# Kernel tuning notes

Hardware: AMD Instinct MI355X
Metric: run time of the kernel (lower is better)

Reference implementation:

```python
import jax, jax.numpy as jnp
from jax import lax
import numpy as np

B, N, C = 16, 2048, 512


def setup_inputs() -> dict:
    key = jax.random.key(0)
    ks = jax.random.split(key, 9)
    s1 = (2.0 / C) ** 0.5   # kaiming fan_in for k=1 convs
    s3 = (2.0 / (3 * C)) ** 0.5  # kaiming fan_in for k=3 convs
    return {
        "x": jax.random.normal(ks[0], (B, N, C), jnp.float32),
        "w1_q": jax.random.normal(ks[1], (C, C), jnp.float32) * s1,
        "w3_q": jax.random.normal(ks[2], (C, C, 3), jnp.float32) * s3,
        "w1_k": jax.random.normal(ks[3], (C, C), jnp.float32) * s1,
        "w3_k": jax.random.normal(ks[4], (C, C, 3), jnp.float32) * s3,
        "w1_v": jax.random.normal(ks[5], (C, C), jnp.float32) * s1,
        "w3_v": jax.random.normal(ks[6], (C, C, 3), jnp.float32) * s3,
        "w_proj": jax.random.normal(ks[7], (C, C), jnp.float32) * s1,
        "b_proj": jax.random.normal(ks[8], (C,), jnp.float32) * 0.01,
    }


def _qkv_branch(xc, w1, w3):
    # xc: [B, C, N]; conv1d k=1 (no bias) then conv1d k=3, circular pad 1 (no bias)
    h = jnp.einsum("oc,bcn->bon", w1, xc)
    hp = jnp.pad(h, ((0, 0), (0, 0), (1, 1)), mode="wrap")
    return lax.conv_general_dilated(
        hp, w3, window_strides=(1,), padding="VALID",
        dimension_numbers=("NCH", "OIH", "NCH"))  # [B, C, N]


def reference(x, w1_q, w3_q, w1_k, w3_k, w1_v, w3_v, w_proj, b_proj):
    # x: [B, N, C]
    xc = jnp.transpose(x, (0, 2, 1))  # [B, C, N]
    q = _qkv_branch(xc, w1_q, w3_q)
    k = _qkv_branch(xc, w1_k, w3_k)
    v = _qkv_branch(xc, w1_v, w3_v)
    # channel attention: scores are [B, C, C]; scale applied twice = 1/d_model
    scale2 = 1.0 / C
    attn = jnp.einsum("bcn,bdn->bcd", q, k) * scale2
    attn = jax.nn.softmax(attn, axis=-1)
    out = jnp.einsum("bcd,bdn->bcn", attn, v)  # [B, C, N]
    y = jnp.einsum("oc,bcn->bon", w_proj, out) + b_proj[None, :, None]
    return jnp.transpose(y, (0, 2, 1))  # [B, N, C]
```

## Files before the change

### kernel.cpp

```cpp
#include <hip/hip_runtime.h>
#include <hip/hip_bf16.h>
#include <hip/hip_fp16.h>
#include <stdint.h>

typedef __bf16 bf16;
typedef __bf16 bf16x8 __attribute__((ext_vector_type(8)));
typedef _Float16 f16x8 __attribute__((ext_vector_type(8)));
typedef float f32x4 __attribute__((ext_vector_type(4)));

#define NSEQ 2048
#define CDIM 512

#define WS_FLAGS   0
#define WS_BPB     1024
#define WS_WPB     4096
#define WS_WEC     532480
#define WS_WECT    3678208
#define WS_W1T     5251072
#define WS_W3R     6823936
#define WS_BASE    11542528

__device__ __forceinline__ float rdf(const void* p, long i, int f) {
  if (f == 1) return ((const float*)p)[i];
  if (f == 2) return (float)((const _Float16*)p)[i];
  return (float)((const bf16*)p)[i];
}

__device__ __forceinline__ void gl_lds16(const bf16* g, bf16* l) {
  __builtin_amdgcn_global_load_lds(
      (__attribute__((address_space(1))) void*)g,
      (__attribute__((address_space(3))) void*)l, 16, 0, 0);
}

__device__ __forceinline__ void stage_one(const void* gb, long eoff, int dt,
                                          bf16* ldst)
{
  if (dt == 1) {
    const float* g = (const float*)gb + eoff;
    const float4 u0 = *(const float4*)g;
    const float4 u1 = *(const float4*)(g + 4);
    bf16x8 t;
    t[0]=(bf16)u0.x; t[1]=(bf16)u0.y; t[2]=(bf16)u0.z; t[3]=(bf16)u0.w;
    t[4]=(bf16)u1.x; t[5]=(bf16)u1.y; t[6]=(bf16)u1.z; t[7]=(bf16)u1.w;
    *(bf16x8*)ldst = t;
  } else if (dt == 2) {
    const f16x8 h = *(const f16x8*)((const _Float16*)gb + eoff);
    bf16x8 t;
#pragma unroll
    for (int j = 0; j < 8; ++j) t[j] = (bf16)(float)h[j];
    *(bf16x8*)ldst = t;
  } else {
    gl_lds16((const bf16*)gb + eoff, ldst);
  }
}

__global__ __launch_bounds__(256)
void detect2(const unsigned short* __restrict__ a,
             const unsigned short* __restrict__ b, int* __restrict__ flags)
{
  const unsigned short* p = blockIdx.x ? b : a;
  __shared__ int chi, clo;
  if (threadIdx.x == 0) { chi = 0; clo = 0; }
  __syncthreads();
  int hi = 0, lo = 0;
  for (int i = threadIdx.x; i < 4096; i += 256) {
    const int e = (p[i] >> 7) & 0xff;
    hi += (e >= 141);
    lo += (e >= 1 && e <= 110);
  }
  atomicAdd(&chi, hi);
  atomicAdd(&clo, lo);
  __syncthreads();
  if (threadIdx.x == 0) {
    flags[blockIdx.x] = (chi > 8) ? 1 : ((clo > 100) ? 2 : 0);
    if (blockIdx.x == 0) flags[2] = 0;
  }
}

__global__ __launch_bounds__(256)
void cvt_x8(const void* __restrict__ x, const int* __restrict__ flag,
            bf16* __restrict__ xb)
{
  const long i8 = (long)blockIdx.x * 256 + threadIdx.x;
  const int f = *flag;
  bf16x8 t;
  if (f == 1) {
    const float4* g = (const float4*)x + i8 * 2;
    const float4 u0 = g[0], u1 = g[1];
    t[0]=(bf16)u0.x; t[1]=(bf16)u0.y; t[2]=(bf16)u0.z; t[3]=(bf16)u0.w;
    t[4]=(bf16)u1.x; t[5]=(bf16)u1.y; t[6]=(bf16)u1.z; t[7]=(bf16)u1.w;
  } else if (f == 2) {
    const f16x8 h = ((const f16x8*)x)[i8];
#pragma unroll
    for (int j = 0; j < 8; ++j) t[j] = (bf16)(float)h[j];
  } else {
    t = ((const bf16x8*)x)[i8];
  }
  ((bf16x8*)xb)[i8] = t;
}

template<int AX3, int BX3, int EPI, int ZMODE>
__global__ __launch_bounds__(256)
void gemm_bt(const void* __restrict__ Abase, const void* __restrict__ Bbase,
             void* __restrict__ Cbase, const bf16* __restrict__ bias,
             const int* __restrict__ xflag, int zxb,
             int M, int Nd, int K, int lda, int ldb, int ldc,
             long zsA, long zsB, long zsC)
{
  __shared__ bf16 As[128 * 32];
  __shared__ bf16 Bs[128 * 32];
  const int z = blockIdx.z;
  const int xdt = (AX3 || BX3) ? *xflag : 0;
  long Aoff, Boff; char* CB;
  if (ZMODE == 1) {
    const int g = z / 3, t = z - g * 3;
    Aoff = (long)z * 262144;
    Boff = (long)g * 262144;
    CB = (char*)Cbase + ((long)g * (512 * 1536) + t * 512) * 2;
  } else {
    Aoff = AX3 ? 0 : (long)z * zsA;
    Boff = BX3 ? 0 : (long)z * zsB;
    CB = (char*)Cbase + (long)z * zsC * (EPI == 2 ? 4 : 2);
  }
  const int m0 = blockIdx.y * 128;
  const int n0 = blockIdx.x * 128;
  const int tid = threadIdx.x;
  const int lane = tid & 63;
  const int w = tid >> 6;
  const int wr = (w >> 1) * 64;
  const int wc = (w & 1) * 64;

  f32x4 acc[4][4];
  const f32x4 zero = {0.f, 0.f, 0.f, 0.f};
#pragma unroll
  for (int i = 0; i < 4; ++i)
#pragma unroll
    for (int j = 0; j < 4; ++j) acc[i][j] = zero;

  for (int k0 = 0; k0 < K; k0 += 32) {
#pragma unroll
    for (int it = 0; it < 2; ++it) {
      const int f  = (it * 256 + tid) * 16;
      const int r  = f >> 6;
      const int cb = (f & 63) >> 1;
      long ea, eb;
      if (AX3) {
        const int tau = k0 >> 9;
        ea = (long)(z + zxb) * zsA +
             (long)((m0 + r + tau - 1) & (NSEQ - 1)) * CDIM + (k0 & 511) + cb;
      } else {
        ea = Aoff + (long)(m0 + r) * lda + k0 + cb;
      }
      stage_one(Abase, ea, AX3 ? xdt : 0, (bf16*)((char*)As + f));
      if (BX3) {
        const int tau = k0 >> 9;
        eb = (long)(z + zxb) * zsB +
             (long)((n0 + r + tau - 1) & (NSEQ - 1)) * CDIM + (k0 & 511) + cb;
      } else {
        eb = Boff + (long)(n0 + r) * ldb + k0 + cb;
      }
      stage_one(Bbase, eb, BX3 ? xdt : 0, (bf16*)((char*)Bs + f));
    }
    __syncthreads();

    const int qb = (lane >> 4) * 16;
    const int fr = lane & 15;
    bf16x8 af[4], bfr[4];
#pragma unroll
    for (int i = 0; i < 4; ++i)
      af[i] = *(const bf16x8*)((const char*)As + (wr + i * 16 + fr) * 64 + qb);
#pragma unroll
    for (int j = 0; j < 4; ++j)
      bfr[j] = *(const bf16x8*)((const char*)Bs + (wc + j * 16 + fr) * 64 + qb);
#pragma unroll
    for (int i = 0; i < 4; ++i)
#pragma unroll
      for (int j = 0; j < 4; ++j)
        acc[i][j] = __builtin_amdgcn_mfma_f32_16x16x32_bf16(af[i], bfr[j], acc[i][j], 0, 0, 0);
    __syncthreads();
  }

  const int qa4 = (lane >> 4) * 4;
  const int cn = lane & 15;
#pragma unroll
  for (int i = 0; i < 4; ++i) {
#pragma unroll
    for (int j = 0; j < 4; ++j) {
      const int gn = n0 + wc + j * 16 + cn;
      const float bv = (EPI == 2) ? (float)bias[gn] : 0.f;
#pragma unroll
      for (int r = 0; r < 4; ++r) {
        const long gm = m0 + wr + i * 16 + qa4 + r;
        if (EPI == 2) ((float*)CB)[gm * ldc + gn] = acc[i][j][r] + bv;
        else          ((bf16*)CB)[gm * ldc + gn] = (bf16)acc[i][j][r];
      }
    }
  }
}

template<int X3>
__device__ __forceinline__ void stage32(const bf16* __restrict__ gb, long zoff,
                                        int r0, int k0, int ld,
                                        char* ldsb, int tid)
{
#pragma unroll
  for (int is = 0; is < 2; ++is) {
    const int c = is * 512 + tid;
    const int g = c >> 6;
    const int l = c & 63;
    const int r = g * 16 + (l & 15);
    const int kb = l >> 4;
    long e;
    if (X3) {
      const int tau = k0 >> 9;
      const int rg = (r0 + r + tau - 1) & (NSEQ - 1);
      e = zoff + (long)rg * CDIM + ((k0 & 511) + kb * 8);
    } else {
      e = zoff + (long)(r0 + r) * ld + k0 + kb * 8;
    }
    gl_lds16(gb + e, (bf16*)(ldsb + c * 16));
  }
}

template<int AX3, int BX3, int EPI>
__global__ __launch_bounds__(512)
void gemm8(const bf16* __restrict__ Ab, const bf16* __restrict__ Bb,
           void* __restrict__ Cbase, const bf16* __restrict__ bias,
           int zxb, int M, int Nd, int K, int lda, int ldb, int ldc,
           long zsA, long zsB, long zsC)
{
  __shared__ char smem[65536];
  const int z = blockIdx.z;
  const long Aoff = (long)(AX3 ? (z + zxb) : z) * zsA;
  const long Boff = (long)(BX3 ? (z + zxb) : z) * zsB;
  char* CB = (char*)Cbase + (long)z * zsC * (EPI == 2 ? 4 : 2);
  const int m0 = blockIdx.y * 256;
  const int n0 = blockIdx.x * 256;
  const int tid = threadIdx.x;
  const int lane = tid & 63;
  const int w = tid >> 6, wm = w >> 2, wn = w & 3;
  const int fro = lane * 16;

  f32x4 acc[8][4];
  const f32x4 zero = {0.f, 0.f, 0.f, 0.f};
#pragma unroll
  for (int i = 0; i < 8; ++i)
#pragma unroll
    for (int j = 0; j < 4; ++j) acc[i][j] = zero;

  const int KT = K >> 5;
  stage32<AX3>(Ab, Aoff, m0, 0, lda, smem, tid);
  stage32<BX3>(Bb, Boff, n0, 0, ldb, smem + 16384, tid);
  __syncthreads();

  for (int T = 0; T < KT; ++T) {
    const int cur = T & 1;
    const char* sA = smem + cur * 32768;
    const char* sB = sA + 16384;
    if (T + 1 < KT) {
      char* nb = smem + (cur ^ 1) * 32768;
      const int k1 = (T + 1) << 5;
      stage32<AX3>(Ab, Aoff, m0, k1, lda, nb, tid);
      stage32<BX3>(Bb, Boff, n0, k1, ldb, nb + 16384, tid);
    }
    bf16x8 bfr[4];
#pragma unroll
    for (int j = 0; j < 4; ++j)
      bfr[j] = *(const bf16x8*)(sB + (wn * 4 + j) * 1024 + fro);
#pragma unroll
    for (int h = 0; h < 2; ++h) {
      bf16x8 af[4];
#pragma unroll
      for (int i2 = 0; i2 < 4; ++i2)
        af[i2] = *(const bf16x8*)(sA + (wm * 8 + h * 4 + i2) * 1024 + fro);
      __builtin_amdgcn_s_setprio(1);
#pragma unroll
      for (int i2 = 0; i2 < 4; ++i2)
#pragma unroll
        for (int j = 0; j < 4; ++j)
          acc[h * 4 + i2][j] = __builtin_amdgcn_mfma_f32_16x16x32_bf16(
              af[i2], bfr[j], acc[h * 4 + i2][j], 0, 0, 0);
      __builtin_amdgcn_s_setprio(0);
      if (h == 0) __builtin_amdgcn_s_barrier();
    }
    __syncthreads();
  }

  const int lr = lane & 15, lk = lane >> 4;
#pragma unroll
  for (int i = 0; i < 8; ++i) {
#pragma unroll
    for (int j = 0; j < 4; ++j) {
      const int gn = n0 + wn * 64 + j * 16 + lr;
      const float bv = (EPI == 2) ? (float)bias[gn] : 0.f;
#pragma unroll
      for (int r = 0; r < 4; ++r) {
        const long gm = m0 + wm * 128 + i * 16 + lk * 4 + r;
        if (EPI == 2) ((float*)CB)[gm * ldc + gn] = acc[i][j][r] + bv;
        else          ((bf16*)CB)[gm * ldc + gn] = (bf16)acc[i][j][r];
      }
    }
  }
}

template<int AX3, int BX3, int EPI>
__global__ __launch_bounds__(512)
void gemm8p(const bf16* __restrict__ Ab, const bf16* __restrict__ Bb,
            void* __restrict__ Cbase, const bf16* __restrict__ bias,
            int zxb, int M, int Nd, int K, int lda, int ldb, int ldc,
            long zsA, long zsB, long zsC)
{
  extern __shared__ char smem[];
  const int gx = gridDim.x, gy = gridDim.y;
  const int total = gx * gy * gridDim.z;
  const int lin = blockIdx.x + gx * (blockIdx.y + gy * blockIdx.z);
  const int q = total >> 3, r = total & 7;
  const int xcd = lin & 7, k = lin >> 3;
  int swz = (xcd < r ? xcd * (q + 1) : r * (q + 1) + (xcd - r) * q) + k;
  const int ny = swz % gy; swz /= gy;
  const int nx = swz % gx;
  const int z  = swz / gx;

  const long Aoff = (long)(AX3 ? (z + zxb) : z) * zsA;
  const long Boff = (long)(BX3 ? (z + zxb) : z) * zsB;
  char* CB = (char*)Cbase + (long)z * zsC * (EPI == 2 ? 4 : 2);
  const int m0 = ny * 256;
  const int n0 = nx * 256;
  const int tid = threadIdx.x;
  const int lane = tid & 63;
  const int w = tid >> 6, wm = w >> 2, wn = w & 3;
  const int fro = lane * 16;

  f32x4 acc[8][4];
  const f32x4 zero = {0.f, 0.f, 0.f, 0.f};
#pragma unroll
  for (int i = 0; i < 8; ++i)
#pragma unroll
    for (int j = 0; j < 4; ++j) acc[i][j] = zero;

  const int KT = K >> 5;

  stage32<AX3>(Ab, Aoff, m0, 0, lda, smem, tid);
  stage32<BX3>(Bb, Boff, n0, 0, ldb, smem + 16384, tid);
  stage32<AX3>(Ab, Aoff, m0, 32, lda, smem + 32768, tid);
  stage32<BX3>(Bb, Boff, n0, 32, ldb, smem + 32768 + 16384, tid);

  for (int T = 0; T < KT; ++T) {
    if (T + 1 < KT) asm volatile("s_waitcnt vmcnt(4)" ::: "memory");
    else            asm volatile("s_waitcnt vmcnt(0)" ::: "memory");
    __builtin_amdgcn_s_barrier();

    if (T + 2 < KT) {
      char* nb = smem + ((T + 2) % 3) * 32768;
      const int k2 = (T + 2) << 5;
      stage32<AX3>(Ab, Aoff, m0, k2, lda, nb, tid);
      stage32<BX3>(Bb, Boff, n0, k2, ldb, nb + 16384, tid);
    }

    const char* sA = smem + (T % 3) * 32768;
    const char* sB = sA + 16384;
    bf16x8 bfr[4];
#pragma unroll
    for (int j = 0; j < 4; ++j)
      bfr[j] = *(const bf16x8*)(sB + (wn * 4 + j) * 1024 + fro);
#pragma unroll
    for (int h = 0; h < 2; ++h) {
      bf16x8 af[4];
#pragma unroll
      for (int i2 = 0; i2 < 4; ++i2)
        af[i2] = *(const bf16x8*)(sA + (wm * 8 + h * 4 + i2) * 1024 + fro);
      __builtin_amdgcn_s_setprio(1);
#pragma unroll
      for (int i2 = 0; i2 < 4; ++i2)
#pragma unroll
        for (int j = 0; j < 4; ++j)
          acc[h * 4 + i2][j] = __builtin_amdgcn_mfma_f32_16x16x32_bf16(
              af[i2], bfr[j], acc[h * 4 + i2][j], 0, 0, 0);
      __builtin_amdgcn_s_setprio(0);
      if (h == 0) __builtin_amdgcn_s_barrier();
    }
  }

  const int lr = lane & 15, lk = lane >> 4;
#pragma unroll
  for (int i = 0; i < 8; ++i) {
#pragma unroll
    for (int j = 0; j < 4; ++j) {
      const int gn = n0 + wn * 64 + j * 16 + lr;
      const float bv = (EPI == 2) ? (float)bias[gn] : 0.f;
#pragma unroll
      for (int r2 = 0; r2 < 4; ++r2) {
        const long gm = m0 + wm * 128 + i * 16 + lk * 4 + r2;
        if (EPI == 2) ((float*)CB)[gm * ldc + gn] = acc[i][j][r2] + bv;
        else          ((bf16*)CB)[gm * ldc + gn] = (bf16)acc[i][j][r2];
      }
    }
  }
}

__global__ __launch_bounds__(256)
void repack(const void* __restrict__ w1q, const void* __restrict__ w3q,
            const void* __restrict__ w1k, const void* __restrict__ w3k,
            const void* __restrict__ w1v, const void* __restrict__ w3v,
            const void* __restrict__ wp, const void* __restrict__ bpr,
            const int* __restrict__ flag,
            bf16* __restrict__ w1t, bf16* __restrict__ w3r,
            bf16* __restrict__ wpb, bf16* __restrict__ bpb)
{
  const int isf = *flag;
  const int g = blockIdx.z;
  const void* w1 = (g == 0) ? w1q : (g == 1) ? w1k : w1v;
  const void* w3 = (g == 0) ? w3q : (g == 1) ? w3k : w3v;
  const int idx = blockIdx.x * 256 + threadIdx.x;
  const int o = idx >> 9, c = idx & 511;
  w1t[g * 262144 + idx] = (bf16)rdf(w1, (long)c * 512 + o, isf);
#pragma unroll
  for (int t = 0; t < 3; ++t)
    w3r[(g * 3 + t) * 262144 + idx] = (bf16)rdf(w3, ((long)o * 512 + c) * 3 + t, isf);
  if (g == 0) {
    wpb[idx] = (bf16)rdf(wp, idx, isf);
    if (idx < 512) bpb[idx] = (bf16)rdf(bpr, idx, isf);
  }
}

__global__ __launch_bounds__(256)
void softmax_p1(const bf16* __restrict__ S, float2* __restrict__ P)
{
  const int z = blockIdx.z;
  const int c = blockIdx.x * 256 + threadIdx.x;
  const int d0 = blockIdx.y * 128;
  const bf16* s = S + (long)z * 262144 + c;
  const float sc = 1.0f / 512.0f;
  float m = -3.4e38f, l = 0.f;
  for (int d = d0; d < d0 + 128; ++d) {
    const float v = (float)s[d * 512] * sc;
    const float nm = fmaxf(m, v);
    l = l * __expf(m - nm) + __expf(v - nm);
    m = nm;
  }
  P[((long)z * 4 + blockIdx.y) * 512 + c] = make_float2(m, l);
}

__global__ __launch_bounds__(256)
void softmax_p2(bf16* __restrict__ S, const float2* __restrict__ P)
{
  const int z = blockIdx.z;
  const int c = blockIdx.x * 256 + threadIdx.x;
  const int d0 = blockIdx.y * 128;
  float m = -3.4e38f, l = 0.f;
#pragma unroll
  for (int i = 0; i < 4; ++i) {
    const float2 p = P[((long)z * 4 + i) * 512 + c];
    const float nm = fmaxf(m, p.x);
    l = l * __expf(m - nm) + p.y * __expf(p.x - nm);
    m = nm;
  }
  const float inv = 1.0f / l;
  bf16* s = S + (long)z * 262144 + c;
  const float sc = 1.0f / 512.0f;
  for (int d = d0; d < d0 + 128; ++d) {
    const float v = (float)s[d * 512] * sc;
    s[d * 512] = (bf16)(__expf(v - m) * inv);
  }
}

extern "C" void kernel_launch(void* const* d_in, const int* in_sizes, int n_in,
                              void* d_out, int out_size, void* d_ws, size_t ws_size,
                              hipStream_t stream)
{
  long smax = -1, smin = (long)1 << 62;
  for (int i = 0; i < n_in; ++i) {
    const long s = in_sizes[i];
    if (s > smax) smax = s;
    if (s < smin) smin = s;
  }
  long s3 = -1;
  for (int i = 0; i < n_in; ++i) {
    const long s = in_sizes[i];
    if (s < smax && s > s3) s3 = s;
  }
  int xi = -1, bi = -1, w1i[8], n1 = 0, w3i[8], n3 = 0;
  for (int i = 0; i < n_in; ++i) {
    const long s = in_sizes[i];
    if (s == smax && xi < 0) xi = i;
    else if (s == smin && bi < 0) bi = i;
    else if (s == s3) { if (n3 < 8) w3i[n3++] = i; }
    else             { if (n1 < 8) w1i[n1++] = i; }
  }
  const void *x, *w1q, *w3q, *w1k, *w3k, *w1v, *w3v, *wp, *bp;
  if (xi >= 0 && bi >= 0 && n1 >= 4 && n3 >= 3) {
    x = d_in[xi]; bp = d_in[bi];
    w1q = d_in[w1i[0]]; w1k = d_in[w1i[1]]; w1v = d_in[w1i[2]]; wp = d_in[w1i[3]];
    w3q = d_in[w3i[0]]; w3k = d_in[w3i[1]]; w3v = d_in[w3i[2]];
  } else {
    x = d_in[0]; w1q = d_in[1]; w3q = d_in[2]; w1k = d_in[3]; w3k = d_in[4];
    w1v = d_in[5]; w3v = d_in[6]; wp = d_in[7]; bp = d_in[8];
  }
  float* out = (float*)d_out;

  char* ws = (char*)d_ws;
  int*  flags = (int*)(ws + WS_FLAGS);
  bf16* bpb  = (bf16*)(ws + WS_BPB);
  bf16* wpb  = (bf16*)(ws + WS_WPB);
  bf16* wec  = (bf16*)(ws + WS_WEC);
  bf16* wecT = (bf16*)(ws + WS_WECT);
  bf16* w1t  = (bf16*)(ws + WS_W1T);
  bf16* w3r  = (bf16*)(ws + WS_W3R);

  int NB = 16, conv = 1;
  while (NB >= 1 && WS_BASE + (size_t)NB * 2621440 + 33554432 > ws_size) NB >>= 1;
  if (NB == 0) {
    conv = 0; NB = 16;
    while (NB > 1 && WS_BASE + (size_t)NB * 2621440 > ws_size) NB >>= 1;
  }
  bf16* Sb    = (bf16*)(ws + WS_BASE);
  bf16* slotA = (bf16*)(ws + WS_BASE + (size_t)NB * 524288);
  bf16* U     = slotA;
  bf16* Wfin  = slotA + (size_t)NB * 262144;
  bf16* xb    = (bf16*)(ws + WS_BASE + (size_t)NB * 2621440);
  float2* Pp  = (float2*)slotA;

  const dim3 blk(256, 1, 1);
  const dim3 blk8(512, 1, 1);

  bool ok8 = true;
  {
    hipError_t e;
    e = hipFuncSetAttribute(reinterpret_cast<const void*>(&gemm8p<0, 1, 0>),
                            hipFuncAttributeMaxDynamicSharedMemorySize, 98304);
    ok8 = ok8 && (e == hipSuccess);
    e = hipFuncSetAttribute(reinterpret_cast<const void*>(&gemm8p<0, 0, 0>),
                            hipFuncAttributeMaxDynamicSharedMemorySize, 98304);
    ok8 = ok8 && (e == hipSuccess);
    e = hipFuncSetAttribute(reinterpret_cast<const void*>(&gemm8p<1, 0, 2>),
                            hipFuncAttributeMaxDynamicSharedMemorySize, 98304);
    ok8 = ok8 && (e == hipSuccess);
  }

  detect2<<<dim3(2, 1, 1), blk, 0, stream>>>(
      (const unsigned short*)x, (const unsigned short*)w1q, flags);

  const void* xu = x;
  const int* xflag = flags;
  if (conv) {
    cvt_x8<<<dim3(8192, 1, 1), blk, 0, stream>>>(x, flags, xb);
    xu = xb;
    xflag = flags + 2;
  }

  repack<<<dim3(1024, 1, 3), blk, 0, stream>>>(w1q, w3q, w1k, w3k, w1v, w3v,
                                               wp, bp, flags + 1,
                                               w1t, w3r, wpb, bpb);
  gemm_bt<0, 0, 0, 1><<<dim3(4, 4, 6), blk, 0, stream>>>(
      w3r, w1t, wec, nullptr, nullptr, 0, 512, 512, 512, 512, 512, 1536, 0, 0, 0);
  gemm_bt<0, 0, 0, 0><<<dim3(4, 4, 3), blk, 0, stream>>>(
      w1t + 2 * 262144, w3r + 6 * 262144, wecT, nullptr, nullptr, 0,
      512, 512, 512, 512, 512, 512, 0, 262144, 262144);

  for (int b0 = 0; b0 < 16; b0 += NB) {
    char* outc = (char*)out + (size_t)b0 * 2048 * 512 * 4;
    if (conv) {
      bf16* QKc = (bf16*)outc;
      if (ok8) {
        gemm8p<0, 1, 0><<<dim3(8, 4, NB), blk8, 98304, stream>>>(
            wec, (const bf16*)xu, QKc, nullptr, b0,
            1024, 2048, 1536, 1536, 0, 2048,
            0, (long)NSEQ * CDIM, (long)1024 * 2048);
      } else {
        gemm8<0, 1, 0><<<dim3(8, 4, NB), blk8, 0, stream>>>(
            wec, (const bf16*)xu, QKc, nullptr, b0,
            1024, 2048, 1536, 1536, 0, 2048,
            0, (long)NSEQ * CDIM, (long)1024 * 2048);
      }
      gemm_bt<0, 0, 0, 0><<<dim3(4, 4, NB), blk, 0, stream>>>(
          QKc + (long)512 * 2048, QKc, Sb, nullptr, nullptr, 0,
          512, 512, 2048, 2048, 2048, 512,
          (long)1024 * 2048, (long)1024 * 2048, (long)512 * 512);
      softmax_p1<<<dim3(2, 4, NB), blk, 0, stream>>>(Sb, Pp);
      softmax_p2<<<dim3(2, 4, NB), blk, 0, stream>>>(Sb, Pp);
      gemm_bt<0, 0, 0, 0><<<dim3(4, 4, NB), blk, 0, stream>>>(
          wpb, Sb, U, nullptr, nullptr, 0, 512, 512, 512, 512, 512, 512,
          0, (long)512 * 512, (long)512 * 512);
      if (ok8) {
        gemm8p<0, 0, 0><<<dim3(6, 2, NB), blk8, 98304, stream>>>(
            U, wecT, Wfin, nullptr, 0, 512, 1536, 512, 512, 512, 1536,
            (long)512 * 512, 0, (long)512 * 1536);
        gemm8p<1, 0, 2><<<dim3(2, 8, NB), blk8, 98304, stream>>>(
            (const bf16*)xu, Wfin, outc, bpb, b0,
            2048, 512, 1536, 0, 1536, 512,
            (long)NSEQ * CDIM, (long)512 * 1536, (long)2048 * 512);
      } else {
        gemm8<0, 0, 0><<<dim3(6, 2, NB), blk8, 0, stream>>>(
            U, wecT, Wfin, nullptr, 0, 512, 1536, 512, 512, 512, 1536,
            (long)512 * 512, 0, (long)512 * 1536);
        gemm8<1, 0, 2><<<dim3(2, 8, NB), blk8, 0, stream>>>(
            (const bf16*)xu, Wfin, outc, bpb, b0,
            2048, 512, 1536, 0, 1536, 512,
            (long)NSEQ * CDIM, (long)512 * 1536, (long)2048 * 512);
      }
    } else {
      bf16* Kc = (bf16*)outc;
      gemm_bt<0, 1, 0, 0><<<dim3(16, 4, NB), blk, 0, stream>>>(
          wec, xu, slotA, nullptr, xflag, b0, 512, 2048, 1536, 1536, 0, 2048,
          0, (long)NSEQ * CDIM, (long)512 * 2048);
      gemm_bt<0, 1, 0, 0><<<dim3(16, 4, NB), blk, 0, stream>>>(
          wec + 512 * 1536, xu, Kc, nullptr, xflag, b0, 512, 2048, 1536, 1536, 0, 2048,
          0, (long)NSEQ * CDIM, (long)512 * 2048);
      gemm_bt<0, 0, 0, 0><<<dim3(4, 4, NB), blk, 0, stream>>>(
          Kc, slotA, Sb, nullptr, nullptr, 0, 512, 512, 2048, 2048, 2048, 512,
          (long)512 * 2048, (long)512 * 2048, (long)512 * 512);
      softmax_p1<<<dim3(2, 4, NB), blk, 0, stream>>>(Sb, Pp);
      softmax_p2<<<dim3(2, 4, NB), blk, 0, stream>>>(Sb, Pp);
      gemm_bt<0, 0, 0, 0><<<dim3(4, 4, NB), blk, 0, stream>>>(
          wpb, Sb, U, nullptr, nullptr, 0, 512, 512, 512, 512, 512, 512,
          0, (long)512 * 512, (long)512 * 512);
      gemm_bt<0, 0, 0, 0><<<dim3(12, 4, NB), blk, 0, stream>>>(
          U, wecT, Wfin, nullptr, nullptr, 0, 512, 1536, 512, 512, 512, 1536,
          (long)512 * 512, 0, (long)512 * 1536);
      gemm_bt<1, 0, 2, 0><<<dim3(4, 16, NB), blk, 0, stream>>>(
          xu, Wfin, outc, bpb, xflag, b0,
          2048, 512, 1536, 0, 1536, 512,
          (long)NSEQ * CDIM, (long)512 * 1536, (long)2048 * 512);
    }
  }
}
```

Measured before the change: 437.9 us.

## Switch swizzled GEMM to 32x32x16 MFMA with matching LDS staging layout

```diff
diff --git a/kernel.cpp b/kernel.cpp
--- a/kernel.cpp
+++ b/kernel.cpp
@@ -7,6 +7,7 @@
 typedef __bf16 bf16x8 __attribute__((ext_vector_type(8)));
 typedef _Float16 f16x8 __attribute__((ext_vector_type(8)));
 typedef float f32x4 __attribute__((ext_vector_type(4)));
+typedef float f32x16 __attribute__((ext_vector_type(16)));
 
 #define NSEQ 2048
 #define CDIM 512
@@ -222,6 +223,28 @@
   }
 }
 
+template<int X3>
+__device__ __forceinline__ void stage32w(const bf16* __restrict__ gb, long zoff,
+                                         int r0, int k0, int ld,
+                                         char* ldsb, int tid)
+{
+#pragma unroll
+  for (int is = 0; is < 2; ++is) {
+    const int c = is * 512 + tid;
+    const int r = ((c >> 7) << 5) | (c & 31);
+    const int kb = (c >> 5) & 3;
+    long e;
+    if (X3) {
+      const int tau = k0 >> 9;
+      const int rg = (r0 + r + tau - 1) & (NSEQ - 1);
+      e = zoff + (long)rg * CDIM + ((k0 & 511) + kb * 8);
+    } else {
+      e = zoff + (long)(r0 + r) * ld + k0 + kb * 8;
+    }
+    gl_lds16(gb + e, (bf16*)(ldsb + c * 16));
+  }
+}
+
 template<int AX3, int BX3, int EPI>
 __global__ __launch_bounds__(512)
 void gemm8(const bf16* __restrict__ Ab, const bf16* __restrict__ Bb,
@@ -331,19 +354,20 @@
   const int w = tid >> 6, wm = w >> 2, wn = w & 3;
   const int fro = lane * 16;
 
-  f32x4 acc[8][4];
-  const f32x4 zero = {0.f, 0.f, 0.f, 0.f};
-#pragma unroll
-  for (int i = 0; i < 8; ++i)
-#pragma unroll
-    for (int j = 0; j < 4; ++j) acc[i][j] = zero;
+  f32x16 acc[4][2];
+#pragma unroll
+  for (int i = 0; i < 4; ++i)
+#pragma unroll
+    for (int j = 0; j < 2; ++j)
+#pragma unroll
+      for (int e = 0; e < 16; ++e) acc[i][j][e] = 0.f;
 
   const int KT = K >> 5;
 
-  stage32<AX3>(Ab, Aoff, m0, 0, lda, smem, tid);
-  stage32<BX3>(Bb, Boff, n0, 0, ldb, smem + 16384, tid);
-  stage32<AX3>(Ab, Aoff, m0, 32, lda, smem + 32768, tid);
-  stage32<BX3>(Bb, Boff, n0, 32, ldb, smem + 32768 + 16384, tid);
+  stage32w<AX3>(Ab, Aoff, m0, 0, lda, smem, tid);
+  stage32w<BX3>(Bb, Boff, n0, 0, ldb, smem + 16384, tid);
+  stage32w<AX3>(Ab, Aoff, m0, 32, lda, smem + 32768, tid);
+  stage32w<BX3>(Bb, Boff, n0, 32, ldb, smem + 32768 + 16384, tid);
 
   for (int T = 0; T < KT; ++T) {
     if (T + 1 < KT) asm volatile("s_waitcnt vmcnt(4)" ::: "memory");
@@ -353,46 +377,49 @@
     if (T + 2 < KT) {
       char* nb = smem + ((T + 2) % 3) * 32768;
       const int k2 = (T + 2) << 5;
-      stage32<AX3>(Ab, Aoff, m0, k2, lda, nb, tid);
-      stage32<BX3>(Bb, Boff, n0, k2, ldb, nb + 16384, tid);
+      stage32w<AX3>(Ab, Aoff, m0, k2, lda, nb, tid);
+      stage32w<BX3>(Bb, Boff, n0, k2, ldb, nb + 16384, tid);
     }
 
     const char* sA = smem + (T % 3) * 32768;
     const char* sB = sA + 16384;
-    bf16x8 bfr[4];
-#pragma unroll
-    for (int j = 0; j < 4; ++j)
-      bfr[j] = *(const bf16x8*)(sB + (wn * 4 + j) * 1024 + fro);
-#pragma unroll
-    for (int h = 0; h < 2; ++h) {
-      bf16x8 af[4];
-#pragma unroll
-      for (int i2 = 0; i2 < 4; ++i2)
-        af[i2] = *(const bf16x8*)(sA + (wm * 8 + h * 4 + i2) * 1024 + fro);
-      __builtin_amdgcn_s_setprio(1);
-#pragma unroll
-      for (int i2 = 0; i2 < 4; ++i2)
-#pragma unroll
-        for (int j = 0; j < 4; ++j)
-          acc[h * 4 + i2][j] = __builtin_amdgcn_mfma_f32_16x16x32_bf16(
-              af[i2], bfr[j], acc[h * 4 + i2][j], 0, 0, 0);
-      __builtin_amdgcn_s_setprio(0);
-      if (h == 0) __builtin_amdgcn_s_barrier();
-    }
-  }
-
-  const int lr = lane & 15, lk = lane >> 4;
-#pragma unroll
-  for (int i = 0; i < 8; ++i) {
-#pragma unroll
-    for (int j = 0; j < 4; ++j) {
-      const int gn = n0 + wn * 64 + j * 16 + lr;
+    bf16x8 bfr[2][2], af[4][2];
+#pragma unroll
+    for (int nb2 = 0; nb2 < 2; ++nb2)
+#pragma unroll
+      for (int ks = 0; ks < 2; ++ks)
+        bfr[nb2][ks] = *(const bf16x8*)(sB + (wn * 2 + nb2) * 2048 + ks * 1024 + fro);
+#pragma unroll
+    for (int mb = 0; mb < 4; ++mb)
+#pragma unroll
+      for (int ks = 0; ks < 2; ++ks)
+        af[mb][ks] = *(const bf16x8*)(sA + (wm * 4 + mb) * 2048 + ks * 1024 + fro);
+
+    __builtin_amdgcn_s_setprio(1);
+#pragma unroll
+    for (int mb = 0; mb < 4; ++mb)
+#pragma unroll
+      for (int nb2 = 0; nb2 < 2; ++nb2)
+#pragma unroll
+        for (int ks = 0; ks < 2; ++ks)
+          acc[mb][nb2] = __builtin_amdgcn_mfma_f32_32x32x16_bf16(
+              af[mb][ks], bfr[nb2][ks], acc[mb][nb2], 0, 0, 0);
+    __builtin_amdgcn_s_setprio(0);
+  }
+
+  const int cn = lane & 31;
+  const int l5 = (lane >> 5) * 4;
+#pragma unroll
+  for (int mb = 0; mb < 4; ++mb) {
+#pragma unroll
+    for (int nb2 = 0; nb2 < 2; ++nb2) {
+      const int gn = n0 + wn * 64 + nb2 * 32 + cn;
       const float bv = (EPI == 2) ? (float)bias[gn] : 0.f;
 #pragma unroll
-      for (int r2 = 0; r2 < 4; ++r2) {
-        const long gm = m0 + wm * 128 + i * 16 + lk * 4 + r2;
-        if (EPI == 2) ((float*)CB)[gm * ldc + gn] = acc[i][j][r2] + bv;
-        else          ((bf16*)CB)[gm * ldc + gn] = (bf16)acc[i][j][r2];
+      for (int reg = 0; reg < 16; ++reg) {
+        const long gm = m0 + wm * 128 + mb * 32 + (reg & 3) + 8 * (reg >> 2) + l5;
+        if (EPI == 2) ((float*)CB)[gm * ldc + gn] = acc[mb][nb2][reg] + bv;
+        else          ((bf16*)CB)[gm * ldc + gn] = (bf16)acc[mb][nb2][reg];
       }
     }
   }
```

After: 443.6 us. Within noise of the previous version (+1.3%).

## Replace triple-buffered K32 GEMM pipeline with double-buffered K64 stages

Applied to the files above, without the earlier changes.

```diff
diff --git a/kernel.cpp b/kernel.cpp
--- a/kernel.cpp
+++ b/kernel.cpp
@@ -303,20 +303,39 @@
   }
 }
 
+template<int X3>
+__device__ __forceinline__ void issue8(const bf16* __restrict__ gb, long zoff,
+                                       int r0, int k0, int ld, char* ldsb,
+                                       const int* rowT, const int* kT, int tid)
+{
+#pragma unroll
+  for (int it = 0; it < 4; ++it) {
+    long e;
+    if (X3) {
+      const int tau = k0 >> 9;
+      const int rg = (r0 + rowT[it] + tau - 1) & (NSEQ - 1);
+      e = zoff + (long)rg * CDIM + ((k0 & 511) + kT[it]);
+    } else {
+      e = zoff + (long)(r0 + rowT[it]) * ld + k0 + kT[it];
+    }
+    gl_lds16(gb + e, (bf16*)(ldsb + (it * 512 + tid) * 16));
+  }
+}
+
 template<int AX3, int BX3, int EPI>
 __global__ __launch_bounds__(512)
-void gemm8p(const bf16* __restrict__ Ab, const bf16* __restrict__ Bb,
-            void* __restrict__ Cbase, const bf16* __restrict__ bias,
-            int zxb, int M, int Nd, int K, int lda, int ldb, int ldc,
-            long zsA, long zsB, long zsC)
+void gemm9(const bf16* __restrict__ Ab, const bf16* __restrict__ Bb,
+           void* __restrict__ Cbase, const bf16* __restrict__ bias,
+           int zxb, int M, int Nd, int K, int lda, int ldb, int ldc,
+           long zsA, long zsB, long zsC)
 {
   extern __shared__ char smem[];
   const int gx = gridDim.x, gy = gridDim.y;
   const int total = gx * gy * gridDim.z;
   const int lin = blockIdx.x + gx * (blockIdx.y + gy * blockIdx.z);
   const int q = total >> 3, r = total & 7;
-  const int xcd = lin & 7, k = lin >> 3;
-  int swz = (xcd < r ? xcd * (q + 1) : r * (q + 1) + (xcd - r) * q) + k;
+  const int xcd = lin & 7, kq = lin >> 3;
+  int swz = (xcd < r ? xcd * (q + 1) : r * (q + 1) + (xcd - r) * q) + kq;
   const int ny = swz % gy; swz /= gy;
   const int nx = swz % gx;
   const int z  = swz / gx;
@@ -331,6 +350,15 @@
   const int w = tid >> 6, wm = w >> 2, wn = w & 3;
   const int fro = lane * 16;
 
+  int rowT[4], kT[4];
+#pragma unroll
+  for (int it = 0; it < 4; ++it) {
+    const int c2 = it * 512 + tid;
+    const int blk = c2 >> 6, l = c2 & 63;
+    rowT[it] = ((blk >> 1) << 4) + (l & 15);
+    kT[it]   = ((blk & 1) << 5) + ((l >> 4) << 3);
+  }
+
   f32x4 acc[8][4];
   const f32x4 zero = {0.f, 0.f, 0.f, 0.f};
 #pragma unroll
@@ -338,46 +366,53 @@
 #pragma unroll
     for (int j = 0; j < 4; ++j) acc[i][j] = zero;
 
-  const int KT = K >> 5;
-
-  stage32<AX3>(Ab, Aoff, m0, 0, lda, smem, tid);
-  stage32<BX3>(Bb, Boff, n0, 0, ldb, smem + 16384, tid);
-  stage32<AX3>(Ab, Aoff, m0, 32, lda, smem + 32768, tid);
-  stage32<BX3>(Bb, Boff, n0, 32, ldb, smem + 32768 + 16384, tid);
+  const int KT = K >> 6;
+
+  issue8<AX3>(Ab, Aoff, m0, 0, lda, smem, rowT, kT, tid);
+  issue8<BX3>(Bb, Boff, n0, 0, ldb, smem + 32768, rowT, kT, tid);
+  asm volatile("s_waitcnt vmcnt(0)" ::: "memory");
+  __builtin_amdgcn_s_barrier();
 
   for (int T = 0; T < KT; ++T) {
-    if (T + 1 < KT) asm volatile("s_waitcnt vmcnt(4)" ::: "memory");
-    else            asm volatile("s_waitcnt vmcnt(0)" ::: "memory");
-    __builtin_amdgcn_s_barrier();
-
-    if (T + 2 < KT) {
-      char* nb = smem + ((T + 2) % 3) * 32768;
-      const int k2 = (T + 2) << 5;
-      stage32<AX3>(Ab, Aoff, m0, k2, lda, nb, tid);
-      stage32<BX3>(Bb, Boff, n0, k2, ldb, nb + 16384, tid);
-    }
-
-    const char* sA = smem + (T % 3) * 32768;
-    const char* sB = sA + 16384;
-    bf16x8 bfr[4];
+    const char* sA = smem + (T & 1) * 65536;
+    const char* sB = sA + 32768;
+    char* nb = smem + ((T + 1) & 1) * 65536;
+    const int k1 = (T + 1) << 6;
+    const bool st = (T + 1 < KT);
+
+    bf16x8 bfr[4][2];
 #pragma unroll
     for (int j = 0; j < 4; ++j)
-      bfr[j] = *(const bf16x8*)(sB + (wn * 4 + j) * 1024 + fro);
-#pragma unroll
-    for (int h = 0; h < 2; ++h) {
-      bf16x8 af[4];
-#pragma unroll
-      for (int i2 = 0; i2 < 4; ++i2)
-        af[i2] = *(const bf16x8*)(sA + (wm * 8 + h * 4 + i2) * 1024 + fro);
+#pragma unroll
+      for (int s = 0; s < 2; ++s)
+        bfr[j][s] = *(const bf16x8*)(sB + (((wn * 4 + j) * 2 + s) << 10) + fro);
+
+#pragma unroll
+    for (int p = 0; p < 4; ++p) {
+      bf16x8 af[2][2];
+#pragma unroll
+      for (int i2 = 0; i2 < 2; ++i2)
+#pragma unroll
+        for (int s = 0; s < 2; ++s)
+          af[i2][s] = *(const bf16x8*)(
+              sA + (((wm * 8 + 2 * p + i2) * 2 + s) << 10) + fro);
+      if (p == 0 && st) {
+        issue8<AX3>(Ab, Aoff, m0, k1, lda, nb, rowT, kT, tid);
+        issue8<BX3>(Bb, Boff, n0, k1, ldb, nb + 32768, rowT, kT, tid);
+      }
+      __builtin_amdgcn_s_barrier();
       __builtin_amdgcn_s_setprio(1);
 #pragma unroll
-      for (int i2 = 0; i2 < 4; ++i2)
-#pragma unroll
-        for (int j = 0; j < 4; ++j)
-          acc[h * 4 + i2][j] = __builtin_amdgcn_mfma_f32_16x16x32_bf16(
-              af[i2], bfr[j], acc[h * 4 + i2][j], 0, 0, 0);
+      for (int s = 0; s < 2; ++s)
+#pragma unroll
+        for (int i2 = 0; i2 < 2; ++i2)
+#pragma unroll
+          for (int j = 0; j < 4; ++j)
+            acc[2 * p + i2][j] = __builtin_amdgcn_mfma_f32_16x16x32_bf16(
+                af[i2][s], bfr[j][s], acc[2 * p + i2][j], 0, 0, 0);
       __builtin_amdgcn_s_setprio(0);
-      if (h == 0) __builtin_amdgcn_s_barrier();
+      if (p == 3 && st) asm volatile("s_waitcnt vmcnt(0)" ::: "memory");
+      __builtin_amdgcn_s_barrier();
     }
   }
 
@@ -523,18 +558,18 @@
   const dim3 blk(256, 1, 1);
   const dim3 blk8(512, 1, 1);
 
-  bool ok8 = true;
+  bool ok9 = true;
   {
     hipError_t e;
-    e = hipFuncSetAttribute(reinterpret_cast<const void*>(&gemm8p<0, 1, 0>),
-                            hipFuncAttributeMaxDynamicSharedMemorySize, 98304);
-    ok8 = ok8 && (e == hipSuccess);
-    e = hipFuncSetAttribute(reinterpret_cast<const void*>(&gemm8p<0, 0, 0>),
-                            hipFuncAttributeMaxDynamicSharedMemorySize, 98304);
-    ok8 = ok8 && (e == hipSuccess);
-    e = hipFuncSetAttribute(reinterpret_cast<const void*>(&gemm8p<1, 0, 2>),
-                            hipFuncAttributeMaxDynamicSharedMemorySize, 98304);
-    ok8 = ok8 && (e == hipSuccess);
+    e = hipFuncSetAttribute(reinterpret_cast<const void*>(&gemm9<0, 1, 0>),
+                            hipFuncAttributeMaxDynamicSharedMemorySize, 131072);
+    ok9 = ok9 && (e == hipSuccess);
+    e = hipFuncSetAttribute(reinterpret_cast<const void*>(&gemm9<0, 0, 0>),
+                            hipFuncAttributeMaxDynamicSharedMemorySize, 131072);
+    ok9 = ok9 && (e == hipSuccess);
+    e = hipFuncSetAttribute(reinterpret_cast<const void*>(&gemm9<1, 0, 2>),
+                            hipFuncAttributeMaxDynamicSharedMemorySize, 131072);
+    ok9 = ok9 && (e == hipSuccess);
   }
 
   detect2<<<dim3(2, 1, 1), blk, 0, stream>>>(
@@ -561,8 +596,8 @@
     char* outc = (char*)out + (size_t)b0 * 2048 * 512 * 4;
     if (conv) {
       bf16* QKc = (bf16*)outc;
-      if (ok8) {
-        gemm8p<0, 1, 0><<<dim3(8, 4, NB), blk8, 98304, stream>>>(
+      if (ok9) {
+        gemm9<0, 1, 0><<<dim3(8, 4, NB), blk8, 131072, stream>>>(
             wec, (const bf16*)xu, QKc, nullptr, b0,
             1024, 2048, 1536, 1536, 0, 2048,
             0, (long)NSEQ * CDIM, (long)1024 * 2048);
@@ -581,11 +616,11 @@
       gemm_bt<0, 0, 0, 0><<<dim3(4, 4, NB), blk, 0, stream>>>(
           wpb, Sb, U, nullptr, nullptr, 0, 512, 512, 512, 512, 512, 512,
           0, (long)512 * 512, (long)512 * 512);
-      if (ok8) {
-        gemm8p<0, 0, 0><<<dim3(6, 2, NB), blk8, 98304, stream>>>(
+      if (ok9) {
+        gemm9<0, 0, 0><<<dim3(6, 2, NB), blk8, 131072, stream>>>(
             U, wecT, Wfin, nullptr, 0, 512, 1536, 512, 512, 512, 1536,
             (long)512 * 512, 0, (long)512 * 1536);
-        gemm8p<1, 0, 2><<<dim3(2, 8, NB), blk8, 98304, stream>>>(
+        gemm9<1, 0, 2><<<dim3(2, 8, NB), blk8, 131072, stream>>>(
             (const bf16*)xu, Wfin, outc, bpb, b0,
             2048, 512, 1536, 0, 1536, 512,
             (long)NSEQ * CDIM, (long)512 * 1536, (long)2048 * 512);
```

Measured after the change: 480.5 us. 1.1x slower.
